# Kernel tuning notes

Measured on AMD Instinct MI355X. Metric: run time of the kernel, lower is better.

Reference implementation:

```python
import jax, jax.numpy as jnp
import numpy as np

DIM = 4096
BATCH = 8192
NUM_LAYERS = 6
STRENGTHS = (0.1, 0.1, 0.05)  # entail, contra, neutral
EPS_NORM = 1e-12  # torch F.normalize eps
MAX_NORM = 10.0


def _normalize(x, axis=-1):
    n = jnp.linalg.norm(x, axis=axis, keepdims=True)
    return x / jnp.maximum(n, EPS_NORM)


def setup_inputs() -> dict:
    key = jax.random.key(0)
    k0, k1, k2, k3 = jax.random.split(key, 4)
    return {
        "h0": jax.random.normal(k0, (BATCH, DIM), dtype=jnp.float32),
        "anchor_entail": jax.random.normal(k1, (DIM,), dtype=jnp.float32),
        "anchor_contra": jax.random.normal(k2, (DIM,), dtype=jnp.float32),
        "anchor_neutral": jax.random.normal(k3, (DIM,), dtype=jnp.float32),
    }


def reference(h0, anchor_entail, anchor_contra, anchor_neutral):
    # Normalized fixed anchor directions, stacked [3, dim] (E, C, N)
    dirs = jnp.stack([
        _normalize(anchor_entail, axis=0),
        _normalize(anchor_contra, axis=0),
        _normalize(anchor_neutral, axis=0),
    ])  # [3, dim]
    strengths = jnp.asarray(STRENGTHS, dtype=h0.dtype)  # [3]

    def step(h, _):
        h_n = _normalize(h)                         # [B, dim]
        align = jnp.einsum("bd,kd->bk", h_n, dirs)  # [B, 3]
        div = 1.0 - align                           # divergence_from_alignment
        tens = jnp.maximum(div, 0.0)                # tension (clamp min=0)
        # normalized direction away from each anchor: [B, 3, dim]
        vec = _normalize(h[:, None, :] - dirs[None, :, :])
        force = jnp.einsum("bk,bkd->bd", strengths[None, :] * div, vec)
        h = h - force
        h_norm = jnp.linalg.norm(h, axis=-1, keepdims=True)
        h = jnp.where(h_norm > MAX_NORM, h * (MAX_NORM / (h_norm + 1e-8)), h)
        return h, (align, div, tens)

    h_final, (aligns, divs, tensions) = jax.lax.scan(step, h0, None, length=NUM_LAYERS)
    # traces: [num_layers, B, 3] with anchor order (entail, contra, neutral)
    return h_final, aligns, divs, tensions
```

## Files before the change

### kernel.cpp

```cpp
#include <hip/hip_runtime.h>


constexpr int DIM = 4096;
constexpr int BATCH = 8192;
constexpr int NLAYERS = 6;
constexpr int TPB = 256;
constexpr int VPT = DIM / (TPB * 4);

constexpr size_t HOUT = (size_t)BATCH * DIM;
constexpr size_t TRACE = (size_t)NLAYERS * BATCH * 3;
constexpr size_t OFF_ALIGN = HOUT;
constexpr size_t OFF_DIV   = HOUT + TRACE;
constexpr size_t OFF_TENS  = HOUT + 2 * TRACE;

__device__ float  g_gram[16];
__device__ float4 g_dots[BATCH];
__device__ float4 g_coef[BATCH];

__device__ __forceinline__ float wave_red(float v) {
#pragma unroll
  for (int off = 32; off > 0; off >>= 1) v += __shfl_down(v, off, 64);
  return v;
}

__global__ __launch_bounds__(TPB) void dots_kernel(
    const float* __restrict__ h0,
    const float* __restrict__ an0, const float* __restrict__ an1,
    const float* __restrict__ an2) {
  const int tid = threadIdx.x;
  const int b = blockIdx.x;
  const int lane = tid & 63, wv = tid >> 6;
  __shared__ float lds[4][6];

  if (b == BATCH) {
    float r[6];
#pragma unroll
    for (int i = 0; i < 6; ++i) r[i] = 0.f;
#pragma unroll
    for (int j = 0; j < VPT; ++j) {
      const int idx = (tid + j * TPB) * 4;
      const float4 x = *(const float4*)(an0 + idx);
      const float4 y = *(const float4*)(an1 + idx);
      const float4 z = *(const float4*)(an2 + idx);
      r[0] += x.x*x.x + x.y*x.y + x.z*x.z + x.w*x.w;
      r[1] += y.x*y.x + y.y*y.y + y.z*y.z + y.w*y.w;
      r[2] += z.x*z.x + z.y*z.y + z.z*z.z + z.w*z.w;
      r[3] += x.x*y.x + x.y*y.y + x.z*y.z + x.w*y.w;
      r[4] += x.x*z.x + x.y*z.y + x.z*z.z + x.w*z.w;
      r[5] += y.x*z.x + y.y*z.y + y.z*z.z + y.w*z.w;
    }
#pragma unroll
    for (int i = 0; i < 6; ++i) r[i] = wave_red(r[i]);
    if (lane == 0) {
#pragma unroll
      for (int i = 0; i < 6; ++i) lds[wv][i] = r[i];
    }
    __syncthreads();
    if (tid == 0) {
#pragma unroll
      for (int i = 0; i < 6; ++i)
        r[i] = lds[0][i] + lds[1][i] + lds[2][i] + lds[3][i];
      const float n0 = fmaxf(sqrtf(r[0]), 1e-12f);
      const float n1 = fmaxf(sqrtf(r[1]), 1e-12f);
      const float n2 = fmaxf(sqrtf(r[2]), 1e-12f);
      g_gram[0] = n0; g_gram[1] = n1; g_gram[2] = n2;
      g_gram[3] = r[3] / (n0 * n1);
      g_gram[4] = r[4] / (n0 * n2);
      g_gram[5] = r[5] / (n1 * n2);
      g_gram[6] = r[0] / (n0 * n0);
      g_gram[7] = r[1] / (n1 * n1);
      g_gram[8] = r[2] / (n2 * n2);
    }
    return;
  }

  const float* hrow = h0 + (size_t)b * DIM;
  float r[4] = {0.f, 0.f, 0.f, 0.f};
#pragma unroll
  for (int j = 0; j < VPT; ++j) {
    const int idx = (tid + j * TPB) * 4;
    const float4 h = *(const float4*)(hrow + idx);
    const float4 x = *(const float4*)(an0 + idx);
    const float4 y = *(const float4*)(an1 + idx);
    const float4 z = *(const float4*)(an2 + idx);
    r[0] += h.x*h.x + h.y*h.y + h.z*h.z + h.w*h.w;
    r[1] += h.x*x.x + h.y*x.y + h.z*x.z + h.w*x.w;
    r[2] += h.x*y.x + h.y*y.y + h.z*y.z + h.w*y.w;
    r[3] += h.x*z.x + h.y*z.y + h.z*z.z + h.w*z.w;
  }
#pragma unroll
  for (int i = 0; i < 4; ++i) r[i] = wave_red(r[i]);
  if (lane == 0) {
#pragma unroll
    for (int i = 0; i < 4; ++i) lds[wv][i] = r[i];
  }
  __syncthreads();
  if (tid == 0) {
    g_dots[b] = make_float4(lds[0][0] + lds[1][0] + lds[2][0] + lds[3][0],
                            lds[0][1] + lds[1][1] + lds[2][1] + lds[3][1],
                            lds[0][2] + lds[1][2] + lds[2][2] + lds[3][2],
                            lds[0][3] + lds[1][3] + lds[2][3] + lds[3][3]);
  }
}

__global__ __launch_bounds__(TPB) void recur_kernel(float* __restrict__ out) {
  const int b = blockIdx.x * TPB + threadIdx.x;
  const float4 dt = g_dots[b];

  const float n0 = g_gram[0], n1 = g_gram[1], n2 = g_gram[2];
  float G[3][3];
  G[0][1] = G[1][0] = g_gram[3];
  G[0][2] = G[2][0] = g_gram[4];
  G[1][2] = G[2][1] = g_gram[5];
  G[0][0] = g_gram[6]; G[1][1] = g_gram[7]; G[2][2] = g_gram[8];

  const float str[3] = {0.1f, 0.1f, 0.05f};
  float s = dt.x;
  float d[3] = {dt.y / n0, dt.z / n1, dt.w / n2};
  float A = 1.f;
  float B[3] = {0.f, 0.f, 0.f};

#pragma unroll
  for (int l = 0; l < NLAYERS; ++l) {
    const float hn = fmaxf(sqrtf(s), 1e-12f);
    float al[3], dv[3], c[3];
#pragma unroll
    for (int k = 0; k < 3; ++k) {
      al[k] = d[k] / hn;
      dv[k] = 1.f - al[k];
      const float rr = fmaxf(sqrtf(s - 2.f * d[k] + G[k][k]), 1e-12f);
      c[k] = str[k] * dv[k] / rr;
    }
#pragma unroll
    for (int k = 0; k < 3; ++k) {
      const size_t o = (size_t)l * (BATCH * 3) + (size_t)b * 3 + k;
      out[OFF_ALIGN + o] = al[k];
      out[OFF_DIV + o]   = dv[k];
      out[OFF_TENS + o]  = fmaxf(dv[k], 0.f);
    }
    const float a = 1.f - (c[0] + c[1] + c[2]);
    float dn[3];
#pragma unroll
    for (int j = 0; j < 3; ++j)
      dn[j] = a * d[j] + c[0] * G[0][j] + c[1] * G[1][j] + c[2] * G[2][j];
    float sn = a * a * s + 2.f * a * (c[0]*d[0] + c[1]*d[1] + c[2]*d[2]);
#pragma unroll
    for (int k = 0; k < 3; ++k)
#pragma unroll
      for (int j = 0; j < 3; ++j) sn += c[k] * c[j] * G[k][j];
    A = a * A;
#pragma unroll
    for (int j = 0; j < 3; ++j) B[j] = a * B[j] + c[j];
    s = sn;
#pragma unroll
    for (int j = 0; j < 3; ++j) d[j] = dn[j];
    const float hn2 = sqrtf(s);
    if (hn2 > 10.0f) {
      const float sc = 10.0f / (hn2 + 1e-8f);
      A *= sc;
#pragma unroll
      for (int j = 0; j < 3; ++j) { B[j] *= sc; d[j] *= sc; }
      s *= sc * sc;
    }
  }
  g_coef[b] = make_float4(A, B[0] / n0, B[1] / n1, B[2] / n2);
}

__global__ __launch_bounds__(TPB) void apply_kernel(
    const float* __restrict__ h0,
    const float* __restrict__ an0, const float* __restrict__ an1,
    const float* __restrict__ an2, float* __restrict__ out) {
  const int b = blockIdx.x;
  const int tid = threadIdx.x;
  const float4 cf = g_coef[b];
  const float* hrow = h0 + (size_t)b * DIM;
  float* orow = out + (size_t)b * DIM;
#pragma unroll
  for (int j = 0; j < VPT; ++j) {
    const int idx = (tid + j * TPB) * 4;
    const float4 h = *(const float4*)(hrow + idx);
    const float4 x = *(const float4*)(an0 + idx);
    const float4 y = *(const float4*)(an1 + idx);
    const float4 z = *(const float4*)(an2 + idx);
    float4 o;
    o.x = cf.x * h.x + cf.y * x.x + cf.z * y.x + cf.w * z.x;
    o.y = cf.x * h.y + cf.y * x.y + cf.z * y.y + cf.w * z.y;
    o.z = cf.x * h.z + cf.y * x.z + cf.z * y.z + cf.w * z.z;
    o.w = cf.x * h.w + cf.y * x.w + cf.z * y.w + cf.w * z.w;
    *(float4*)(orow + idx) = o;
  }
}

extern "C" void kernel_launch(void* const* d_in, const int* in_sizes, int n_in,
                              void* d_out, int out_size, void* d_ws, size_t ws_size,
                              hipStream_t stream) {
  const float* h0  = (const float*)d_in[0];
  const float* an0 = (const float*)d_in[1];
  const float* an1 = (const float*)d_in[2];
  const float* an2 = (const float*)d_in[3];
  float* out = (float*)d_out;
  (void)d_ws; (void)ws_size;
  dots_kernel<<<BATCH + 1, TPB, 0, stream>>>(h0, an0, an1, an2);
  recur_kernel<<<BATCH / TPB, TPB, 0, stream>>>(out);
  apply_kernel<<<BATCH, TPB, 0, stream>>>(h0, an0, an1, an2, out);
}
```

Measured before the change: 261.2 us.

## Fuse dots, recurrence and apply into one kernel keeping h rows in registers

Merges the three-kernel pipeline into a single per-row kernel. Each block loads its h0 row once into registers, computes row and anchor dot products plus the anchor Gram matrix, runs the closed-form 6-layer recurrence redundantly per thread, and writes the output from the cached row. This removes the second full read of h0 and two kernel launches. In exchange, every block recomputes the anchor Gram and does the serial recurrence inside the memory-bound kernel.

```diff
diff --git a/kernel.cpp b/kernel.cpp
--- a/kernel.cpp
+++ b/kernel.cpp
@@ -13,110 +13,73 @@
 constexpr size_t OFF_DIV   = HOUT + TRACE;
 constexpr size_t OFF_TENS  = HOUT + 2 * TRACE;
 
-__device__ float  g_gram[16];
-__device__ float4 g_dots[BATCH];
-__device__ float4 g_coef[BATCH];
-
 __device__ __forceinline__ float wave_red(float v) {
 #pragma unroll
   for (int off = 32; off > 0; off >>= 1) v += __shfl_down(v, off, 64);
   return v;
 }
 
-__global__ __launch_bounds__(TPB) void dots_kernel(
+__global__ __launch_bounds__(TPB) void fused_kernel(
     const float* __restrict__ h0,
     const float* __restrict__ an0, const float* __restrict__ an1,
-    const float* __restrict__ an2) {
+    const float* __restrict__ an2, float* __restrict__ out) {
+  const int b = blockIdx.x;
   const int tid = threadIdx.x;
-  const int b = blockIdx.x;
   const int lane = tid & 63, wv = tid >> 6;
-  __shared__ float lds[4][6];
+  const float* hrow = h0 + (size_t)b * DIM;
 
-  if (b == BATCH) {
-    float r[6];
+  float4 hv[VPT];
+  float r[10];
 #pragma unroll
-    for (int i = 0; i < 6; ++i) r[i] = 0.f;
-#pragma unroll
-    for (int j = 0; j < VPT; ++j) {
-      const int idx = (tid + j * TPB) * 4;
-      const float4 x = *(const float4*)(an0 + idx);
-      const float4 y = *(const float4*)(an1 + idx);
-      const float4 z = *(const float4*)(an2 + idx);
-      r[0] += x.x*x.x + x.y*x.y + x.z*x.z + x.w*x.w;
-      r[1] += y.x*y.x + y.y*y.y + y.z*y.z + y.w*y.w;
-      r[2] += z.x*z.x + z.y*z.y + z.z*z.z + z.w*z.w;
-      r[3] += x.x*y.x + x.y*y.y + x.z*y.z + x.w*y.w;
-      r[4] += x.x*z.x + x.y*z.y + x.z*z.z + x.w*z.w;
-      r[5] += y.x*z.x + y.y*z.y + y.z*z.z + y.w*z.w;
-    }
-#pragma unroll
-    for (int i = 0; i < 6; ++i) r[i] = wave_red(r[i]);
-    if (lane == 0) {
-#pragma unroll
-      for (int i = 0; i < 6; ++i) lds[wv][i] = r[i];
-    }
-    __syncthreads();
-    if (tid == 0) {
-#pragma unroll
-      for (int i = 0; i < 6; ++i)
-        r[i] = lds[0][i] + lds[1][i] + lds[2][i] + lds[3][i];
-      const float n0 = fmaxf(sqrtf(r[0]), 1e-12f);
-      const float n1 = fmaxf(sqrtf(r[1]), 1e-12f);
-      const float n2 = fmaxf(sqrtf(r[2]), 1e-12f);
-      g_gram[0] = n0; g_gram[1] = n1; g_gram[2] = n2;
-      g_gram[3] = r[3] / (n0 * n1);
-      g_gram[4] = r[4] / (n0 * n2);
-      g_gram[5] = r[5] / (n1 * n2);
-      g_gram[6] = r[0] / (n0 * n0);
-      g_gram[7] = r[1] / (n1 * n1);
-      g_gram[8] = r[2] / (n2 * n2);
-    }
-    return;
-  }
-
-  const float* hrow = h0 + (size_t)b * DIM;
-  float r[4] = {0.f, 0.f, 0.f, 0.f};
+  for (int i = 0; i < 10; ++i) r[i] = 0.f;
 #pragma unroll
   for (int j = 0; j < VPT; ++j) {
     const int idx = (tid + j * TPB) * 4;
-    const float4 h = *(const float4*)(hrow + idx);
+    hv[j] = *(const float4*)(hrow + idx);
     const float4 x = *(const float4*)(an0 + idx);
     const float4 y = *(const float4*)(an1 + idx);
     const float4 z = *(const float4*)(an2 + idx);
+    const float4 h = hv[j];
     r[0] += h.x*h.x + h.y*h.y + h.z*h.z + h.w*h.w;
     r[1] += h.x*x.x + h.y*x.y + h.z*x.z + h.w*x.w;
     r[2] += h.x*y.x + h.y*y.y + h.z*y.z + h.w*y.w;
     r[3] += h.x*z.x + h.y*z.y + h.z*z.z + h.w*z.w;
+    r[4] += x.x*x.x + x.y*x.y + x.z*x.z + x.w*x.w;
+    r[5] += y.x*y.x + y.y*y.y + y.z*y.z + y.w*y.w;
+    r[6] += z.x*z.x + z.y*z.y + z.z*z.z + z.w*z.w;
+    r[7] += x.x*y.x + x.y*y.y + x.z*y.z + x.w*y.w;
+    r[8] += x.x*z.x + x.y*z.y + x.z*z.z + x.w*z.w;
+    r[9] += y.x*z.x + y.y*z.y + y.z*z.z + y.w*z.w;
   }
+
+  __shared__ float lds[4][10];
 #pragma unroll
-  for (int i = 0; i < 4; ++i) r[i] = wave_red(r[i]);
+  for (int i = 0; i < 10; ++i) r[i] = wave_red(r[i]);
   if (lane == 0) {
 #pragma unroll
-    for (int i = 0; i < 4; ++i) lds[wv][i] = r[i];
+    for (int i = 0; i < 10; ++i) lds[wv][i] = r[i];
   }
   __syncthreads();
-  if (tid == 0) {
-    g_dots[b] = make_float4(lds[0][0] + lds[1][0] + lds[2][0] + lds[3][0],
-                            lds[0][1] + lds[1][1] + lds[2][1] + lds[3][1],
-                            lds[0][2] + lds[1][2] + lds[2][2] + lds[3][2],
-                            lds[0][3] + lds[1][3] + lds[2][3] + lds[3][3]);
-  }
-}
 
-__global__ __launch_bounds__(TPB) void recur_kernel(float* __restrict__ out) {
-  const int b = blockIdx.x * TPB + threadIdx.x;
-  const float4 dt = g_dots[b];
+  float t[10];
+#pragma unroll
+  for (int i = 0; i < 10; ++i)
+    t[i] = lds[0][i] + lds[1][i] + lds[2][i] + lds[3][i];
 
-  const float n0 = g_gram[0], n1 = g_gram[1], n2 = g_gram[2];
+  const float n0 = fmaxf(sqrtf(t[4]), 1e-12f);
+  const float n1 = fmaxf(sqrtf(t[5]), 1e-12f);
+  const float n2 = fmaxf(sqrtf(t[6]), 1e-12f);
   float G[3][3];
-  G[0][1] = G[1][0] = g_gram[3];
-  G[0][2] = G[2][0] = g_gram[4];
-  G[1][2] = G[2][1] = g_gram[5];
-  G[0][0] = g_gram[6]; G[1][1] = g_gram[7]; G[2][2] = g_gram[8];
+  G[0][0] = t[4] / (n0 * n0);
+  G[1][1] = t[5] / (n1 * n1);
+  G[2][2] = t[6] / (n2 * n2);
+  G[0][1] = G[1][0] = t[7] / (n0 * n1);
+  G[0][2] = G[2][0] = t[8] / (n0 * n2);
+  G[1][2] = G[2][1] = t[9] / (n1 * n2);
 
   const float str[3] = {0.1f, 0.1f, 0.05f};
-  float s = dt.x;
-  float d[3] = {dt.y / n0, dt.z / n1, dt.w / n2};
+  float s = t[0];
+  float d[3] = {t[1] / n0, t[2] / n1, t[3] / n2};
   float A = 1.f;
   float B[3] = {0.f, 0.f, 0.f};
 
@@ -131,12 +94,14 @@
       const float rr = fmaxf(sqrtf(s - 2.f * d[k] + G[k][k]), 1e-12f);
       c[k] = str[k] * dv[k] / rr;
     }
+    if (tid == 0) {
 #pragma unroll
-    for (int k = 0; k < 3; ++k) {
-      const size_t o = (size_t)l * (BATCH * 3) + (size_t)b * 3 + k;
-      out[OFF_ALIGN + o] = al[k];
-      out[OFF_DIV + o]   = dv[k];
-      out[OFF_TENS + o]  = fmaxf(dv[k], 0.f);
+      for (int k = 0; k < 3; ++k) {
+        const size_t o = (size_t)l * (BATCH * 3) + (size_t)b * 3 + k;
+        out[OFF_ALIGN + o] = al[k];
+        out[OFF_DIV + o]   = dv[k];
+        out[OFF_TENS + o]  = fmaxf(dv[k], 0.f);
+      }
     }
     const float a = 1.f - (c[0] + c[1] + c[2]);
     float dn[3];
@@ -163,30 +128,21 @@
       s *= sc * sc;
     }
   }
-  g_coef[b] = make_float4(A, B[0] / n0, B[1] / n1, B[2] / n2);
-}
+  const float w0 = B[0] / n0, w1 = B[1] / n1, w2 = B[2] / n2;
 
-__global__ __launch_bounds__(TPB) void apply_kernel(
-    const float* __restrict__ h0,
-    const float* __restrict__ an0, const float* __restrict__ an1,
-    const float* __restrict__ an2, float* __restrict__ out) {
-  const int b = blockIdx.x;
-  const int tid = threadIdx.x;
-  const float4 cf = g_coef[b];
-  const float* hrow = h0 + (size_t)b * DIM;
   float* orow = out + (size_t)b * DIM;
 #pragma unroll
   for (int j = 0; j < VPT; ++j) {
     const int idx = (tid + j * TPB) * 4;
-    const float4 h = *(const float4*)(hrow + idx);
     const float4 x = *(const float4*)(an0 + idx);
     const float4 y = *(const float4*)(an1 + idx);
     const float4 z = *(const float4*)(an2 + idx);
+    const float4 h = hv[j];
     float4 o;
-    o.x = cf.x * h.x + cf.y * x.x + cf.z * y.x + cf.w * z.x;
-    o.y = cf.x * h.y + cf.y * x.y + cf.z * y.y + cf.w * z.y;
-    o.z = cf.x * h.z + cf.y * x.z + cf.z * y.z + cf.w * z.z;
-    o.w = cf.x * h.w + cf.y * x.w + cf.z * y.w + cf.w * z.w;
+    o.x = A * h.x + w0 * x.x + w1 * y.x + w2 * z.x;
+    o.y = A * h.y + w0 * x.y + w1 * y.y + w2 * z.y;
+    o.z = A * h.z + w0 * x.z + w1 * y.z + w2 * z.z;
+    o.w = A * h.w + w0 * x.w + w1 * y.w + w2 * z.w;
     *(float4*)(orow + idx) = o;
   }
 }
@@ -200,7 +156,5 @@
   const float* an2 = (const float*)d_in[3];
   float* out = (float*)d_out;
   (void)d_ws; (void)ws_size;
-  dots_kernel<<<BATCH + 1, TPB, 0, stream>>>(h0, an0, an1, an2);
-  recur_kernel<<<BATCH / TPB, TPB, 0, stream>>>(out);
-  apply_kernel<<<BATCH, TPB, 0, stream>>>(h0, an0, an1, an2, out);
+  fused_kernel<<<BATCH, TPB, 0, stream>>>(h0, an0, an1, an2, out);
 }
```

Result: slower. 272.3 us (+4.2%).
